# Performance work log

Measured on AMD Instinct MI355X. Metric: run time of the kernel, lower is better.

The kernel has to match this reference:

```python
import jax, jax.numpy as jnp
import numpy as np

N = 100000       # num nodes
E = 1000000      # num edges
D_IN = 128       # node_input_dim
H = 128          # hidden_dim
D_E = 32         # edge_input_dim
C = 16           # num_classes


def setup_inputs() -> dict:
    key = jax.random.key(0)
    ks = jax.random.split(key, 8)
    x = jax.random.normal(ks[0], (N, D_IN), dtype=jnp.float32)
    edge_index = jax.random.randint(ks[1], (2, E), 0, N)
    edge_attr = jax.random.normal(ks[2], (E, D_E), dtype=jnp.float32)

    def glorot(k, shape):
        fan = shape[0]
        return (jax.random.normal(k, shape, dtype=jnp.float32) / np.sqrt(fan)).astype(jnp.float32)

    W1 = glorot(ks[3], (D_IN, H)); b1 = jnp.zeros((H,), jnp.float32)
    W2 = glorot(ks[4], (H, H));    b2 = jnp.zeros((H,), jnp.float32)
    W3 = glorot(ks[5], (H, H));    b3 = jnp.zeros((H,), jnp.float32)
    W_fc = glorot(ks[6], (D_E + 2 * H, C)); b_fc = jnp.zeros((C,), jnp.float32)
    return {"x": x, "edge_index": edge_index, "edge_attr": edge_attr,
            "W1": W1, "b1": b1, "W2": W2, "b2": b2, "W3": W3, "b3": b3,
            "W_fc": W_fc, "b_fc": b_fc}


def gcn_conv(h_in, W, b, src, dst, dinv):
    """PyG GCNConv: h = D^-1/2 (A+I) D^-1/2 (h_in @ W) + b.
    Self-loop contribution handled analytically as dinv[i]^2 * h[i]."""
    h = h_in @ W                                      # [N, H]
    norm = dinv[src] * dinv[dst]                      # [E]
    msgs = h[src] * norm[:, None]                     # gather + scale, [E, H]
    agg = jax.ops.segment_sum(msgs, dst, num_segments=N)  # scatter-add
    agg = agg + h * (dinv * dinv)[:, None]            # self-loops
    return agg + b


def reference(x, edge_index, edge_attr, W1, b1, W2, b2, W3, b3, W_fc, b_fc):
    src, dst = edge_index[0], edge_index[1]
    # degree with self-loops (edge_weight = 1), as in PyG gcn_norm
    deg = jax.ops.segment_sum(jnp.ones((E,), jnp.float32), dst, num_segments=N) + 1.0
    dinv = jax.lax.rsqrt(deg)

    h = jax.nn.relu(gcn_conv(x, W1, b1, src, dst, dinv))
    # dropout(p=0.3) is identity in eval mode
    h = jax.nn.relu(gcn_conv(h, W2, b2, src, dst, dinv))
    h = jax.nn.relu(gcn_conv(h, W3, b3, src, dst, dinv))

    edge_features = jnp.concatenate([h[src], h[dst], edge_attr], axis=1)  # [E, 2H+D_E]
    edge_output = edge_features @ W_fc + b_fc                             # [E, C]
    return jax.nn.log_softmax(edge_output, axis=1)
```

## Files before the change

kernel.cpp:

```cpp
#include <hip/hip_runtime.h>
#include <hip/hip_bf16.h>

#define D_IN 128
#define HDIM 128
#define D_E  32
#define NC   16
#define SCAN_CHUNK 2048

typedef __attribute__((ext_vector_type(8))) short short8;
typedef __attribute__((ext_vector_type(4))) float float4v;

__device__ inline short f2bs(float f) {
  __hip_bfloat16 h = (__hip_bfloat16)f;
  return *reinterpret_cast<short*>(&h);
}

__device__ inline float bs2f(short s) {
  unsigned int u = ((unsigned int)(unsigned short)s) << 16;
  float f;
  __builtin_memcpy(&f, &u, 4);
  return f;
}


__global__ __launch_bounds__(256) void count_deg(const int* __restrict__ ei, int* __restrict__ deg, int E) {
  int e = blockIdx.x * 256 + threadIdx.x;
  if (e < E) atomicAdd(&deg[ei[E + e]], 1);
}

__global__ __launch_bounds__(256) void scan_blocksums(const int* __restrict__ deg, int* __restrict__ bsum, int n) {
  __shared__ int red[256];
  int t = threadIdx.x;
  int base = blockIdx.x * SCAN_CHUNK + t * 8;
  int s = 0;
#pragma unroll
  for (int j = 0; j < 8; ++j) {
    int i = base + j;
    if (i < n) s += deg[i];
  }
  red[t] = s;
  __syncthreads();
  for (int off = 128; off > 0; off >>= 1) {
    if (t < off) red[t] += red[t + off];
    __syncthreads();
  }
  if (t == 0) bsum[blockIdx.x] = red[0];
}

__global__ __launch_bounds__(256) void scan_offsets(const int* __restrict__ bsum, int* __restrict__ boff, int nb) {
  __shared__ int s[256];
  int t = threadIdx.x;
  int v = (t < nb) ? bsum[t] : 0;
  s[t] = v;
  __syncthreads();
  for (int off = 1; off < 256; off <<= 1) {
    int u = (t >= off) ? s[t - off] : 0;
    __syncthreads();
    s[t] += u;
    __syncthreads();
  }
  if (t < nb) boff[t] = (t == 0) ? 0 : s[t - 1];
}

__global__ __launch_bounds__(256) void scan_write(const int* __restrict__ deg, const int* __restrict__ boff,
                                                  int* __restrict__ rowptr, float* __restrict__ dinv, int n) {
  __shared__ int red[256];
  int t = threadIdx.x;
  int base = blockIdx.x * SCAN_CHUNK + t * 8;
  int v[8];
  int s = 0;
#pragma unroll
  for (int j = 0; j < 8; ++j) {
    int i = base + j;
    v[j] = (i < n) ? deg[i] : 0;
    s += v[j];
  }
  red[t] = s;
  __syncthreads();
  for (int off = 1; off < 256; off <<= 1) {
    int u = (t >= off) ? red[t - off] : 0;
    __syncthreads();
    red[t] += u;
    __syncthreads();
  }
  int run = red[t] - s + boff[blockIdx.x];
#pragma unroll
  for (int j = 0; j < 8; ++j) {
    int i = base + j;
    if (i < n) {
      rowptr[i] = run;
      dinv[i] = rsqrtf((float)v[j] + 1.0f);
    }
    run += v[j];
  }
}

__global__ __launch_bounds__(256) void fill_csr(const int* __restrict__ ei, const int* __restrict__ rowptr,
                                                int* __restrict__ cursor, int* __restrict__ col, int E) {
  int e = blockIdx.x * 256 + threadIdx.x;
  if (e < E) {
    int d = ei[E + e];
    int pos = atomicAdd(&cursor[d], 1);
    col[rowptr[d] + pos] = ei[e];
  }
}

__global__ __launch_bounds__(256) void repack_w128(const float* __restrict__ W, short* __restrict__ wp) {
  int idx = blockIdx.x * 256 + threadIdx.x;
  if (idx < 16384) {
    int j = idx & 7, lane = (idx >> 3) & 63, t = (idx >> 9) & 7, kc = idx >> 12;
    int k = kc * 32 + (lane >> 4) * 8 + j;
    int nn = t * 16 + (lane & 15);
    wp[idx] = f2bs(W[k * HDIM + nn]);
  }
}

__global__ __launch_bounds__(256) void repack_wcp(const float* __restrict__ Wfc, short* __restrict__ wp) {
  int idx = blockIdx.x * 256 + threadIdx.x;
  if (idx < 4096) {
    int j = idx & 7, lane = (idx >> 3) & 63, t = (idx >> 9) & 1, kc = idx >> 10;
    int k = kc * 32 + (lane >> 4) * 8 + j;
    int nn = t * 16 + (lane & 15);
    float v = (nn < 16) ? Wfc[k * NC + nn] : Wfc[(HDIM + k) * NC + (nn - 16)];
    wp[idx] = f2bs(v);
  }
}

__global__ __launch_bounds__(256) void repack_wea(const float* __restrict__ Wfc, short* __restrict__ wp) {
  int idx = blockIdx.x * 256 + threadIdx.x;
  if (idx < 512) {
    int j = idx & 7, lane = (idx >> 3) & 63;
    int k = (lane >> 4) * 8 + j;
    int nn = lane & 15;
    wp[idx] = f2bs(Wfc[(2 * HDIM + k) * NC + nn]);
  }
}

template<int NCOL, bool FP32IN, bool FP32OUT, bool SCALE>
__global__ __launch_bounds__(256) void gemm_mfma(const void* __restrict__ Xv, const short* __restrict__ wpack,
                                                 void* __restrict__ Yv, const float* __restrict__ dscale, int n) {
  constexpr int NT = NCOL / 16;
  __shared__ short sw[4 * NT * 512];
  int tid = threadIdx.x;
  {
    const float4* wg = (const float4*)wpack;
    float4* sg = (float4*)sw;
    for (int i = tid; i < 4 * NT * 512 / 8; i += 256) sg[i] = wg[i];
  }
  __syncthreads();
  int wave = tid >> 6, lane = tid & 63;
  int quad = lane >> 4;
  int row = blockIdx.x * 64 + wave * 16 + (lane & 15);
  bool rowok = row < n;
  float4v acc[NT];
#pragma unroll
  for (int t = 0; t < NT; ++t) acc[t] = (float4v){0.f, 0.f, 0.f, 0.f};

#pragma unroll
  for (int kc = 0; kc < 4; ++kc) {
    short8 af = {0, 0, 0, 0, 0, 0, 0, 0};
    if (rowok) {
      if (FP32IN) {
        const float* xp = (const float*)Xv + (size_t)row * 128 + kc * 32 + quad * 8;
        float4 x0 = *(const float4*)xp;
        float4 x1 = *(const float4*)(xp + 4);
        af[0] = f2bs(x0.x); af[1] = f2bs(x0.y); af[2] = f2bs(x0.z); af[3] = f2bs(x0.w);
        af[4] = f2bs(x1.x); af[5] = f2bs(x1.y); af[6] = f2bs(x1.z); af[7] = f2bs(x1.w);
      } else {
        af = *(const short8*)((const short*)Xv + (size_t)row * 128 + kc * 32 + quad * 8);
      }
    }
#pragma unroll
    for (int t = 0; t < NT; ++t) {
      short8 bfr = *(const short8*)(sw + (kc * NT + t) * 512 + lane * 8);
      acc[t] = __builtin_amdgcn_mfma_f32_16x16x32_bf16(af, bfr, acc[t], 0, 0, 0);
    }
  }
  int orow0 = blockIdx.x * 64 + wave * 16 + quad * 4;
  float dv[4] = {1.f, 1.f, 1.f, 1.f};
  if constexpr (SCALE) {
#pragma unroll
    for (int r = 0; r < 4; ++r) dv[r] = (orow0 + r < n) ? dscale[orow0 + r] : 0.f;
  }
#pragma unroll
  for (int t = 0; t < NT; ++t) {
    int ocol = t * 16 + (lane & 15);
#pragma unroll
    for (int r = 0; r < 4; ++r) {
      int orow = orow0 + r;
      if (orow < n) {
        float val = acc[t][r];
        if constexpr (SCALE) val *= dv[r];
        if (FP32OUT)
          ((float*)Yv)[(size_t)orow * NCOL + ocol] = val;
        else
          ((__hip_bfloat16*)Yv)[(size_t)orow * NCOL + ocol] = (__hip_bfloat16)val;
      }
    }
  }
}

__global__ __launch_bounds__(256) void agg_vec(const __hip_bfloat16* __restrict__ hs, const float* __restrict__ dinv,
                                               const int* __restrict__ rowptr, const int* __restrict__ deg,
                                               const int* __restrict__ col, const float* __restrict__ bias,
                                               __hip_bfloat16* __restrict__ hout, int N) {
  int tid = threadIdx.x;
  int wave = tid >> 6, lane = tid & 63;
  int q = lane >> 4, ft = lane & 15;
  int i = blockIdx.x * 16 + wave * 4 + q;
  bool ok = i < N;
  int iS = ok ? i : (N - 1);
  int s0 = rowptr[iS];
  int dg = ok ? deg[iS] : 0;
  float di = dinv[iS];
  const short* hb = (const short*)hs;
  short8 selfv = *(const short8*)(hb + (size_t)iS * 128 + ft * 8);
  float acc[8];
#pragma unroll
  for (int j = 0; j < 8; ++j) acc[j] = bs2f(selfv[j]);
  for (int b = 0; b < dg; b += 16) {
    int rem = dg - b;
    int myidx = (ft < rem) ? col[s0 + b + ft] : 0;
#pragma unroll
    for (int k = 0; k < 16; ++k) {
      if (k < rem) {
        int ck = __shfl(myidx, (q << 4) + k);
        short8 r = *(const short8*)(hb + (size_t)ck * 128 + ft * 8);
#pragma unroll
        for (int j = 0; j < 8; ++j) acc[j] += bs2f(r[j]);
      }
    }
  }
  if (ok) {
    float4 b0 = *(const float4*)(bias + ft * 8);
    float4 b1 = *(const float4*)(bias + ft * 8 + 4);
    float bb[8] = {b0.x, b0.y, b0.z, b0.w, b1.x, b1.y, b1.z, b1.w};
    short8 o;
#pragma unroll
    for (int j = 0; j < 8; ++j) {
      float v = fmaxf(fmaf(acc[j], di, bb[j]), 0.f);
      o[j] = f2bs(v);
    }
    *(short8*)((short*)hout + (size_t)i * 128 + ft * 8) = o;
  }
}

__global__ __launch_bounds__(256) void edge_fused(const int* __restrict__ ei, const float* __restrict__ ea,
                                                  const short* __restrict__ wpe, const float* __restrict__ bfc,
                                                  const float* __restrict__ PQ, float* __restrict__ out, int E) {
  __shared__ short sw[512];
  __shared__ float sb[16];
  int tid = threadIdx.x;
  if (tid < 64) ((float4*)sw)[tid] = ((const float4*)wpe)[tid];
  if (tid < 16) sb[tid] = bfc[tid];
  __syncthreads();
  int wave = tid >> 6, lane = tid & 63, quad = lane >> 4;
  int row = blockIdx.x * 64 + wave * 16 + (lane & 15);
  short8 af = {0, 0, 0, 0, 0, 0, 0, 0};
  if (row < E) {
    const float* xp = ea + (size_t)row * D_E + quad * 8;
    float4 x0 = *(const float4*)xp;
    float4 x1 = *(const float4*)(xp + 4);
    af[0] = f2bs(x0.x); af[1] = f2bs(x0.y); af[2] = f2bs(x0.z); af[3] = f2bs(x0.w);
    af[4] = f2bs(x1.x); af[5] = f2bs(x1.y); af[6] = f2bs(x1.z); af[7] = f2bs(x1.w);
  }
  short8 bfr = *(const short8*)(sw + lane * 8);
  float4v acc = (float4v){0.f, 0.f, 0.f, 0.f};
  acc = __builtin_amdgcn_mfma_f32_16x16x32_bf16(af, bfr, acc, 0, 0, 0);
  int c = lane & 15;
  int orow0 = blockIdx.x * 64 + wave * 16 + quad * 4;
  float bb = sb[c];
  float ps[4], pd[4];
#pragma unroll
  for (int r = 0; r < 4; ++r) {
    int orow = orow0 + r;
    int er = (orow < E) ? orow : (E - 1);
    int s = ei[er], d = ei[E + er];
    ps[r] = PQ[(size_t)s * 32 + c];
    pd[r] = PQ[(size_t)d * 32 + 16 + c];
  }
#pragma unroll
  for (int r = 0; r < 4; ++r) {
    float l = acc[r] + bb + ps[r] + pd[r];
    float m = l;
#pragma unroll
    for (int w = 1; w < 16; w <<= 1) m = fmaxf(m, __shfl_xor(m, w));
    float ex = __expf(l - m);
    float sum = ex;
#pragma unroll
    for (int w = 1; w < 16; w <<= 1) sum += __shfl_xor(sum, w);
    float lse = __logf(sum) + m;
    int orow = orow0 + r;
    if (orow < E) out[(size_t)orow * NC + c] = l - lse;
  }
}


extern "C" void kernel_launch(void* const* d_in, const int* in_sizes, int n_in,
                              void* d_out, int out_size, void* d_ws, size_t ws_size,
                              hipStream_t stream) {
  const float* x   = (const float*)d_in[0];
  const int*   ei  = (const int*)d_in[1];
  const float* ea  = (const float*)d_in[2];
  const float* W1  = (const float*)d_in[3];
  const float* b1  = (const float*)d_in[4];
  const float* W2  = (const float*)d_in[5];
  const float* b2  = (const float*)d_in[6];
  const float* W3  = (const float*)d_in[7];
  const float* b3  = (const float*)d_in[8];
  const float* Wfc = (const float*)d_in[9];
  const float* bfc = (const float*)d_in[10];
  float* out = (float*)d_out;
  int N = in_sizes[0] / D_IN;
  int E = in_sizes[1] / 2;

  char* w = (char*)d_ws;
  size_t off = 0;
  auto alloc = [&](size_t bytes) -> char* {
    char* p = w + off;
    off += (bytes + 255) & ~(size_t)255;
    return p;
  };
  __hip_bfloat16* A = (__hip_bfloat16*)alloc((size_t)N * HDIM * 2);
  __hip_bfloat16* B = (__hip_bfloat16*)alloc((size_t)N * HDIM * 2);
  float* PQ     = (float*)alloc((size_t)N * 32 * 4);
  int*   col    = (int*)alloc((size_t)E * 4);
  int*   deg    = (int*)alloc((size_t)N * 4);
  int*   cursor = (int*)alloc((size_t)N * 4);
  float* dinv   = (float*)alloc((size_t)N * 4);
  int*   rowptr = (int*)alloc((size_t)N * 4);
  int*   bsum   = (int*)alloc(1024 * 4);
  int*   boff   = (int*)alloc(1024 * 4);
  short* wp1    = (short*)alloc(16384 * 2);
  short* wp2    = (short*)alloc(16384 * 2);
  short* wp3    = (short*)alloc(16384 * 2);
  short* wpc    = (short*)alloc(4096 * 2);
  short* wpe    = (short*)alloc(512 * 2);

  hipMemsetAsync(deg, 0, (size_t)N * 4, stream);
  hipMemsetAsync(cursor, 0, (size_t)N * 4, stream);

  int eb = (E + 255) / 256;
  int sb = (N + SCAN_CHUNK - 1) / SCAN_CHUNK;
  count_deg<<<eb, 256, 0, stream>>>(ei, deg, E);
  scan_blocksums<<<sb, 256, 0, stream>>>(deg, bsum, N);
  scan_offsets<<<1, 256, 0, stream>>>(bsum, boff, sb);
  scan_write<<<sb, 256, 0, stream>>>(deg, boff, rowptr, dinv, N);
  fill_csr<<<eb, 256, 0, stream>>>(ei, rowptr, cursor, col, E);
  repack_w128<<<64, 256, 0, stream>>>(W1, wp1);
  repack_w128<<<64, 256, 0, stream>>>(W2, wp2);
  repack_w128<<<64, 256, 0, stream>>>(W3, wp3);
  repack_wcp<<<16, 256, 0, stream>>>(Wfc, wpc);
  repack_wea<<<2, 256, 0, stream>>>(Wfc, wpe);

  int gb = (N + 63) / 64;
  int ab = (N + 15) / 16;
  int geb = (E + 63) / 64;
  gemm_mfma<128, true,  false, true ><<<gb, 256, 0, stream>>>(x, wp1, A, dinv, N);
  agg_vec<<<ab, 256, 0, stream>>>(A, dinv, rowptr, deg, col, b1, B, N);
  gemm_mfma<128, false, false, true ><<<gb, 256, 0, stream>>>(B, wp2, A, dinv, N);
  agg_vec<<<ab, 256, 0, stream>>>(A, dinv, rowptr, deg, col, b2, B, N);
  gemm_mfma<128, false, false, true ><<<gb, 256, 0, stream>>>(B, wp3, A, dinv, N);
  agg_vec<<<ab, 256, 0, stream>>>(A, dinv, rowptr, deg, col, b3, B, N);
  gemm_mfma<32,  false, true,  false><<<gb, 256, 0, stream>>>(B, wpc, PQ, nullptr, N);
  edge_fused<<<geb, 256, 0, stream>>>(ei, ea, wpe, bfc, PQ, out, E);
}
```

Baseline: 581.4 us.

## Fuse GCN aggregation with following GEMM and reuse degree-count atomics for CSR fill

Each aggregation kernel now writes its 64 aggregated rows into a swizzled LDS tile and immediately runs the next layer's MFMA GEMM on it. This removes the bf16 round trip of the hidden features through global memory and three kernel launches. The CSR fill now reuses the slot positions returned by the atomic in the degree-count kernel, which removes the second atomic pass and the cursor memset. In exchange there is an extra E-sized epos buffer, and the fused kernel uses more LDS and fewer blocks than the old aggregation launch, which may reduce latency hiding in the gather.

Result: slower. 627.9 us (+8.0%).

```diff
diff --git a/kernel.cpp b/kernel.cpp
--- a/kernel.cpp
+++ b/kernel.cpp
@@ -23,9 +23,10 @@
 }
 
 
-__global__ __launch_bounds__(256) void count_deg(const int* __restrict__ ei, int* __restrict__ deg, int E) {
+__global__ __launch_bounds__(256) void count_deg(const int* __restrict__ ei, int* __restrict__ deg,
+                                                 int* __restrict__ epos, int E) {
   int e = blockIdx.x * 256 + threadIdx.x;
-  if (e < E) atomicAdd(&deg[ei[E + e]], 1);
+  if (e < E) epos[e] = atomicAdd(&deg[ei[E + e]], 1);
 }
 
 __global__ __launch_bounds__(256) void scan_blocksums(const int* __restrict__ deg, int* __restrict__ bsum, int n) {
@@ -96,12 +97,11 @@
 }
 
 __global__ __launch_bounds__(256) void fill_csr(const int* __restrict__ ei, const int* __restrict__ rowptr,
-                                                int* __restrict__ cursor, int* __restrict__ col, int E) {
+                                                const int* __restrict__ epos, int* __restrict__ col, int E) {
   int e = blockIdx.x * 256 + threadIdx.x;
   if (e < E) {
     int d = ei[E + e];
-    int pos = atomicAdd(&cursor[d], 1);
-    col[rowptr[d] + pos] = ei[e];
+    col[rowptr[d] + epos[e]] = ei[e];
   }
 }
 
@@ -136,10 +136,9 @@
   }
 }
 
-template<int NCOL, bool FP32IN, bool FP32OUT, bool SCALE>
-__global__ __launch_bounds__(256) void gemm_mfma(const void* __restrict__ Xv, const short* __restrict__ wpack,
-                                                 void* __restrict__ Yv, const float* __restrict__ dscale, int n) {
-  constexpr int NT = NCOL / 16;
+__global__ __launch_bounds__(256) void gemm_l1(const float* __restrict__ Xv, const short* __restrict__ wpack,
+                                               __hip_bfloat16* __restrict__ Yv, const float* __restrict__ dscale, int n) {
+  constexpr int NT = 8;
   __shared__ short sw[4 * NT * 512];
   int tid = threadIdx.x;
   {
@@ -160,15 +159,11 @@
   for (int kc = 0; kc < 4; ++kc) {
     short8 af = {0, 0, 0, 0, 0, 0, 0, 0};
     if (rowok) {
-      if (FP32IN) {
-        const float* xp = (const float*)Xv + (size_t)row * 128 + kc * 32 + quad * 8;
-        float4 x0 = *(const float4*)xp;
-        float4 x1 = *(const float4*)(xp + 4);
-        af[0] = f2bs(x0.x); af[1] = f2bs(x0.y); af[2] = f2bs(x0.z); af[3] = f2bs(x0.w);
-        af[4] = f2bs(x1.x); af[5] = f2bs(x1.y); af[6] = f2bs(x1.z); af[7] = f2bs(x1.w);
-      } else {
-        af = *(const short8*)((const short*)Xv + (size_t)row * 128 + kc * 32 + quad * 8);
-      }
+      const float* xp = Xv + (size_t)row * 128 + kc * 32 + quad * 8;
+      float4 x0 = *(const float4*)xp;
+      float4 x1 = *(const float4*)(xp + 4);
+      af[0] = f2bs(x0.x); af[1] = f2bs(x0.y); af[2] = f2bs(x0.z); af[3] = f2bs(x0.w);
+      af[4] = f2bs(x1.x); af[5] = f2bs(x1.y); af[6] = f2bs(x1.z); af[7] = f2bs(x1.w);
     }
 #pragma unroll
     for (int t = 0; t < NT; ++t) {
@@ -177,6 +172,96 @@
     }
   }
   int orow0 = blockIdx.x * 64 + wave * 16 + quad * 4;
+  float dv[4];
+#pragma unroll
+  for (int r = 0; r < 4; ++r) dv[r] = (orow0 + r < n) ? dscale[orow0 + r] : 0.f;
+#pragma unroll
+  for (int t = 0; t < NT; ++t) {
+    int ocol = t * 16 + (lane & 15);
+#pragma unroll
+    for (int r = 0; r < 4; ++r) {
+      int orow = orow0 + r;
+      if (orow < n) Yv[(size_t)orow * 128 + ocol] = (__hip_bfloat16)(acc[t][r] * dv[r]);
+    }
+  }
+}
+
+template<int NT, bool FP32OUT, bool SCALE>
+__global__ __launch_bounds__(256) void agg_gemm(const __hip_bfloat16* __restrict__ hs, const float* __restrict__ dinv,
+                                                const int* __restrict__ rowptr, const int* __restrict__ deg,
+                                                const int* __restrict__ col, const float* __restrict__ bias,
+                                                const short* __restrict__ wpack, void* __restrict__ Yv,
+                                                const float* __restrict__ dscale, int n) {
+  __shared__ short sw[4 * NT * 512];
+  __shared__ short st[64 * 128];
+  int tid = threadIdx.x;
+  {
+    const float4* wg = (const float4*)wpack;
+    float4* sg = (float4*)sw;
+    for (int i = tid; i < 4 * NT * 512 / 8; i += 256) sg[i] = wg[i];
+  }
+  int wave = tid >> 6, lane = tid & 63;
+  int q = lane >> 4, ft = lane & 15;
+  const short* hb = (const short*)hs;
+  float4 b0 = *(const float4*)(bias + ft * 8);
+  float4 b1 = *(const float4*)(bias + ft * 8 + 4);
+  float bb[8] = {b0.x, b0.y, b0.z, b0.w, b1.x, b1.y, b1.z, b1.w};
+
+  for (int p = 0; p < 4; ++p) {
+    int rl = wave * 16 + p * 4 + q;
+    int i = blockIdx.x * 64 + rl;
+    bool ok = i < n;
+    int iS = ok ? i : (n - 1);
+    int s0 = rowptr[iS];
+    int dg = ok ? deg[iS] : 0;
+    float di = dinv[iS];
+    short8 selfv = *(const short8*)(hb + (size_t)iS * 128 + ft * 8);
+    float acc[8];
+#pragma unroll
+    for (int j = 0; j < 8; ++j) acc[j] = bs2f(selfv[j]);
+    int mx = dg;
+    mx = max(mx, __shfl_xor(mx, 16));
+    mx = max(mx, __shfl_xor(mx, 32));
+    for (int b = 0; b < mx; b += 16) {
+      int rem = dg - b;
+      int myidx = (ft < rem) ? col[s0 + b + ft] : 0;
+#pragma unroll
+      for (int k = 0; k < 16; ++k) {
+        if (k < rem) {
+          int ck = __shfl(myidx, (q << 4) + k);
+          short8 r = *(const short8*)(hb + (size_t)ck * 128 + ft * 8);
+#pragma unroll
+          for (int j = 0; j < 8; ++j) acc[j] += bs2f(r[j]);
+        }
+      }
+    }
+    short8 o;
+#pragma unroll
+    for (int j = 0; j < 8; ++j) {
+      float v = fmaxf(fmaf(acc[j], di, bb[j]), 0.f);
+      o[j] = ok ? f2bs(v) : (short)0;
+    }
+    int byteoff = rl * 256 + ((ft * 16) ^ ((rl & 7) << 4));
+    *(short8*)((char*)st + byteoff) = o;
+  }
+  __syncthreads();
+
+  int quad = lane >> 4;
+  int rl2 = wave * 16 + (lane & 15);
+  float4v acc2[NT];
+#pragma unroll
+  for (int t = 0; t < NT; ++t) acc2[t] = (float4v){0.f, 0.f, 0.f, 0.f};
+#pragma unroll
+  for (int kc = 0; kc < 4; ++kc) {
+    int c0 = kc * 64 + quad * 16;
+    short8 af = *(const short8*)((const char*)st + rl2 * 256 + (c0 ^ ((rl2 & 7) << 4)));
+#pragma unroll
+    for (int t = 0; t < NT; ++t) {
+      short8 bfr = *(const short8*)(sw + (kc * NT + t) * 512 + lane * 8);
+      acc2[t] = __builtin_amdgcn_mfma_f32_16x16x32_bf16(af, bfr, acc2[t], 0, 0, 0);
+    }
+  }
+  int orow0 = blockIdx.x * 64 + wave * 16 + quad * 4;
   float dv[4] = {1.f, 1.f, 1.f, 1.f};
   if constexpr (SCALE) {
 #pragma unroll
@@ -189,59 +274,14 @@
     for (int r = 0; r < 4; ++r) {
       int orow = orow0 + r;
       if (orow < n) {
-        float val = acc[t][r];
+        float val = acc2[t][r];
         if constexpr (SCALE) val *= dv[r];
         if (FP32OUT)
-          ((float*)Yv)[(size_t)orow * NCOL + ocol] = val;
+          ((float*)Yv)[(size_t)orow * NT * 16 + ocol] = val;
         else
-          ((__hip_bfloat16*)Yv)[(size_t)orow * NCOL + ocol] = (__hip_bfloat16)val;
+          ((__hip_bfloat16*)Yv)[(size_t)orow * NT * 16 + ocol] = (__hip_bfloat16)val;
       }
     }
-  }
-}
-
-__global__ __launch_bounds__(256) void agg_vec(const __hip_bfloat16* __restrict__ hs, const float* __restrict__ dinv,
-                                               const int* __restrict__ rowptr, const int* __restrict__ deg,
-                                               const int* __restrict__ col, const float* __restrict__ bias,
-                                               __hip_bfloat16* __restrict__ hout, int N) {
-  int tid = threadIdx.x;
-  int wave = tid >> 6, lane = tid & 63;
-  int q = lane >> 4, ft = lane & 15;
-  int i = blockIdx.x * 16 + wave * 4 + q;
-  bool ok = i < N;
-  int iS = ok ? i : (N - 1);
-  int s0 = rowptr[iS];
-  int dg = ok ? deg[iS] : 0;
-  float di = dinv[iS];
-  const short* hb = (const short*)hs;
-  short8 selfv = *(const short8*)(hb + (size_t)iS * 128 + ft * 8);
-  float acc[8];
-#pragma unroll
-  for (int j = 0; j < 8; ++j) acc[j] = bs2f(selfv[j]);
-  for (int b = 0; b < dg; b += 16) {
-    int rem = dg - b;
-    int myidx = (ft < rem) ? col[s0 + b + ft] : 0;
-#pragma unroll
-    for (int k = 0; k < 16; ++k) {
-      if (k < rem) {
-        int ck = __shfl(myidx, (q << 4) + k);
-        short8 r = *(const short8*)(hb + (size_t)ck * 128 + ft * 8);
-#pragma unroll
-        for (int j = 0; j < 8; ++j) acc[j] += bs2f(r[j]);
-      }
-    }
-  }
-  if (ok) {
-    float4 b0 = *(const float4*)(bias + ft * 8);
-    float4 b1 = *(const float4*)(bias + ft * 8 + 4);
-    float bb[8] = {b0.x, b0.y, b0.z, b0.w, b1.x, b1.y, b1.z, b1.w};
-    short8 o;
-#pragma unroll
-    for (int j = 0; j < 8; ++j) {
-      float v = fmaxf(fmaf(acc[j], di, bb[j]), 0.f);
-      o[j] = f2bs(v);
-    }
-    *(short8*)((short*)hout + (size_t)i * 128 + ft * 8) = o;
   }
 }
 
@@ -324,9 +364,9 @@
   __hip_bfloat16* A = (__hip_bfloat16*)alloc((size_t)N * HDIM * 2);
   __hip_bfloat16* B = (__hip_bfloat16*)alloc((size_t)N * HDIM * 2);
   float* PQ     = (float*)alloc((size_t)N * 32 * 4);
-  int*   col    = (int*)alloc((size_t)E * 4);
+  int*   col    = (int*)alloc((size_t)E * 4 + 256);
+  int*   epos   = (int*)alloc((size_t)E * 4);
   int*   deg    = (int*)alloc((size_t)N * 4);
-  int*   cursor = (int*)alloc((size_t)N * 4);
   float* dinv   = (float*)alloc((size_t)N * 4);
   int*   rowptr = (int*)alloc((size_t)N * 4);
   int*   bsum   = (int*)alloc(1024 * 4);
@@ -338,15 +378,14 @@
   short* wpe    = (short*)alloc(512 * 2);
 
   hipMemsetAsync(deg, 0, (size_t)N * 4, stream);
-  hipMemsetAsync(cursor, 0, (size_t)N * 4, stream);
 
   int eb = (E + 255) / 256;
   int sb = (N + SCAN_CHUNK - 1) / SCAN_CHUNK;
-  count_deg<<<eb, 256, 0, stream>>>(ei, deg, E);
+  count_deg<<<eb, 256, 0, stream>>>(ei, deg, epos, E);
   scan_blocksums<<<sb, 256, 0, stream>>>(deg, bsum, N);
   scan_offsets<<<1, 256, 0, stream>>>(bsum, boff, sb);
   scan_write<<<sb, 256, 0, stream>>>(deg, boff, rowptr, dinv, N);
-  fill_csr<<<eb, 256, 0, stream>>>(ei, rowptr, cursor, col, E);
+  fill_csr<<<eb, 256, 0, stream>>>(ei, rowptr, epos, col, E);
   repack_w128<<<64, 256, 0, stream>>>(W1, wp1);
   repack_w128<<<64, 256, 0, stream>>>(W2, wp2);
   repack_w128<<<64, 256, 0, stream>>>(W3, wp3);
@@ -354,14 +393,10 @@
   repack_wea<<<2, 256, 0, stream>>>(Wfc, wpe);
 
   int gb = (N + 63) / 64;
-  int ab = (N + 15) / 16;
   int geb = (E + 63) / 64;
-  gemm_mfma<128, true,  false, true ><<<gb, 256, 0, stream>>>(x, wp1, A, dinv, N);
-  agg_vec<<<ab, 256, 0, stream>>>(A, dinv, rowptr, deg, col, b1, B, N);
-  gemm_mfma<128, false, false, true ><<<gb, 256, 0, stream>>>(B, wp2, A, dinv, N);
-  agg_vec<<<ab, 256, 0, stream>>>(A, dinv, rowptr, deg, col, b2, B, N);
-  gemm_mfma<128, false, false, true ><<<gb, 256, 0, stream>>>(B, wp3, A, dinv, N);
-  agg_vec<<<ab, 256, 0, stream>>>(A, dinv, rowptr, deg, col, b3, B, N);
-  gemm_mfma<32,  false, true,  false><<<gb, 256, 0, stream>>>(B, wpc, PQ, nullptr, N);
+  gemm_l1<<<gb, 256, 0, stream>>>(x, wp1, A, dinv, N);
+  agg_gemm<8, false, true ><<<gb, 256, 0, stream>>>(A, dinv, rowptr, deg, col, b1, wp2, B, dinv, N);
+  agg_gemm<8, false, true ><<<gb, 256, 0, stream>>>(B, dinv, rowptr, deg, col, b2, wp3, A, dinv, N);
+  agg_gemm<2, true,  false><<<gb, 256, 0, stream>>>(A, dinv, rowptr, deg, col, b3, wpc, PQ, nullptr, N);
   edge_fused<<<geb, 256, 0, stream>>>(ei, ea, wpe, bfc, PQ, out, E);
 }
```
